# Kernel tuning notes

Hardware: AMD Instinct MI355X
Metric: run time of the kernel (lower is better)

## Reference

```python
import jax, jax.numpy as jnp
import numpy as np

B, T, M, D, H, DK, DV = 2, 1024, 1024, 1024, 16, 64, 64
R = 2 * T + M  # number of relative positions required by rel_shift path


def setup_inputs() -> dict:
    key = jax.random.key(0)
    ks = jax.random.split(key, 11)
    s = 0.02
    return {
        "inputs": jax.random.normal(ks[0], (B, T, D), jnp.float32),
        "attention_mask": jnp.ones((B, T, M + T), jnp.float32),
        "positional_encodings": jax.random.normal(ks[1], (R, D), jnp.float32),
        "memory": jax.random.normal(ks[2], (B, M, D), jnp.float32),
        "Wq": jax.random.normal(ks[3], (D, H * DK), jnp.float32) * s,
        "Wk": jax.random.normal(ks[4], (D, H * DK), jnp.float32) * s,
        "Wv": jax.random.normal(ks[5], (D, H * DV), jnp.float32) * s,
        "Wr": jax.random.normal(ks[6], (D, H * DK), jnp.float32) * s,
        "r_w_bias": jax.random.normal(ks[7], (H, DK), jnp.float32) * s,
        "r_r_bias": jax.random.normal(ks[8], (H, DK), jnp.float32) * s,
        "W_out": jax.random.normal(ks[9], (H * DV, D), jnp.float32) * s,
    }


def _rel_shift(m, attention_length):
    # m: [T_q, T_q + L] -> [T_q, L], TXL relative shift via reshape/slice
    tq, total = m.shape
    x = m.reshape(total, tq)[1:].reshape(tq, total - 1)
    return x[:, :attention_length]


def reference(inputs, attention_mask, positional_encodings, memory,
              Wq, Wk, Wv, Wr, r_w_bias, r_r_bias, W_out):
    b, t, d = inputs.shape
    values = jnp.concatenate([memory, inputs], axis=1)  # [B, L, D]
    L = values.shape[1]
    q = (inputs @ Wq).reshape(b, t, H, DK)
    k = (values @ Wk).reshape(b, L, H, DK)
    v = (values @ Wv).reshape(b, L, H, DV)
    rk = (positional_encodings @ Wr).reshape(-1, H, DK)  # [R, H, DK]
    # content + relative logits (TXL)
    content = jnp.einsum('bthd,bThd->bhtT', q + r_w_bias, k)        # [B,H,T,L]
    rel = jnp.einsum('bthd,rhd->bhtr', q + r_r_bias, rk)            # [B,H,T,R]
    rel = jax.vmap(jax.vmap(lambda m: _rel_shift(m, L)))(rel)       # [B,H,T,L]
    logits = (content + rel) * (DK ** -0.5)
    masked = logits - (1.0 - attention_mask[:, None, :, :]) * 1e30
    w = jax.nn.softmax(masked, axis=-1)
    attn = jnp.einsum('bhtT,bThd->bthd', w, v)                      # [B,T,H,DV]
    return attn.reshape(b, t, H * DV) @ W_out
```

## Files before the change

kernel.cpp:

```cpp
#include <hip/hip_runtime.h>
#include <hip/hip_fp16.h>
#include <stdint.h>

#define Bz 2
#define Tq 1024
#define Mm 1024
#define Hh 16
#define Ll 2048
#define Rr 3072

typedef __attribute__((ext_vector_type(8))) short bf16x8;
typedef __attribute__((ext_vector_type(4))) float f32x4;

typedef __attribute__((address_space(3))) uint8_t lds_u8_t;
typedef __attribute__((address_space(1))) uint8_t glb_u8_t;

__device__ __forceinline__ void gl2lds16(const void* g, void* l) {
  __builtin_amdgcn_global_load_lds((const glb_u8_t*)g, (lds_u8_t*)l, 16, 0, 0);
}

__device__ __forceinline__ unsigned short f2bf(float f) {
  unsigned int u = __builtin_bit_cast(unsigned int, f);
  u = u + 0x7fffu + ((u >> 16) & 1u);
  return (unsigned short)(u >> 16);
}
__device__ __forceinline__ float b2f(unsigned short s) {
  unsigned int u = ((unsigned int)s) << 16;
  return __builtin_bit_cast(float, u);
}

__global__ __launch_bounds__(256) void k_prep2(
    const float* __restrict__ x, const float* __restrict__ mem,
    const float* __restrict__ pos, const float* __restrict__ mask,
    const float* __restrict__ w0, const float* __restrict__ w1,
    const float* __restrict__ w2, const float* __restrict__ w3,
    const float* __restrict__ w4,
    unsigned short* __restrict__ vin, unsigned short* __restrict__ pb,
    unsigned short* __restrict__ mb,
    unsigned short* __restrict__ t0, unsigned short* __restrict__ t1,
    unsigned short* __restrict__ t2, unsigned short* __restrict__ t3,
    unsigned short* __restrict__ t4) {
  __shared__ float tile[64][65];
  int bid = blockIdx.x;
  if (bid < 4096) {
    int idx = bid * 256 + threadIdx.x;
    int e = idx << 2;
    int row = e >> 10, col = e & 1023;
    int b = row >> 11, l = row & 2047;
    const float* s = (l < Mm) ? (mem + (((size_t)b * Mm + l) << 10) + col)
                              : (x + (((size_t)b * Tq + (l - Mm)) << 10) + col);
    float4 v = *(const float4*)s;
    ushort4 o;
    o.x = f2bf(v.x); o.y = f2bf(v.y); o.z = f2bf(v.z); o.w = f2bf(v.w);
    *(ushort4*)(vin + e) = o;
  } else if (bid < 7168) {
    int idx = (bid - 4096) * 256 + threadIdx.x;
    int e = idx << 2;
    float4 v = *(const float4*)(pos + e);
    ushort4 t;
    t.x = f2bf(v.x); t.y = f2bf(v.y); t.z = f2bf(v.z); t.w = f2bf(v.w);
    *(ushort4*)(pb + e) = t;
  } else if (bid < 11264) {
    int idx = (bid - 7168) * 256 + threadIdx.x;
    int e = idx << 2;
    const float BIGM = 1.442695e30f;
    float4 v = *(const float4*)(mask + e);
    ushort4 t;
    t.x = f2bf((1.0f - v.x) * BIGM); t.y = f2bf((1.0f - v.y) * BIGM);
    t.z = f2bf((1.0f - v.z) * BIGM); t.w = f2bf((1.0f - v.w) * BIGM);
    *(ushort4*)(mb + e) = t;
  } else {
    int r3 = bid - 11264;
    int mz = r3 >> 8, rem = r3 & 255;
    const float* W;
    unsigned short* WT;
    switch (mz) {
      case 0: W = w0; WT = t0; break;
      case 1: W = w1; WT = t1; break;
      case 2: W = w2; WT = t2; break;
      case 3: W = w3; WT = t3; break;
      default: W = w4; WT = t4; break;
    }
    int k0 = (rem >> 4) * 64, n0 = (rem & 15) * 64;
    int tid = threadIdx.x;
    int rr = tid >> 4, c4 = (tid & 15) * 4;
#pragma unroll
    for (int it = 0; it < 4; ++it) {
      int r = rr + it * 16;
      float4 v = *(const float4*)(W + (size_t)(k0 + r) * 1024 + n0 + c4);
      tile[r][c4] = v.x; tile[r][c4 + 1] = v.y;
      tile[r][c4 + 2] = v.z; tile[r][c4 + 3] = v.w;
    }
    __syncthreads();
#pragma unroll
    for (int it = 0; it < 4; ++it) {
      int n = rr + it * 16;
      ushort4 o;
      o.x = f2bf(tile[c4 + 0][n]); o.y = f2bf(tile[c4 + 1][n]);
      o.z = f2bf(tile[c4 + 2][n]); o.w = f2bf(tile[c4 + 3][n]);
      *(ushort4*)(WT + (size_t)(n0 + n) * 1024 + k0 + c4) = o;
    }
  }
}

template <int RMAP>
__device__ __forceinline__ void gemm_pipe(const unsigned short* __restrict__ A,
                                          const unsigned short* __restrict__ Bt,
                                          int m0, int n0, unsigned short* As,
                                          unsigned short* Bs, f32x4 acc[4][4]) {
  const int tid = threadIdx.x;
  const int w = tid >> 6, lane = tid & 63;
  const int quad = lane >> 4, li = lane & 15;
  const int wr = w >> 1, wc = w & 1;
  f32x4 z = {0.f, 0.f, 0.f, 0.f};
#pragma unroll
  for (int mi = 0; mi < 4; ++mi)
#pragma unroll
    for (int ni = 0; ni < 4; ++ni) acc[mi][ni] = z;

  const int rs = lane >> 2;
  const int cs = lane & 3;

#pragma unroll
  for (int s = 0; s < 2; ++s) {
    int i = w * 2 + s;
    int r = i * 16 + rs;
    int c = cs ^ ((r >> 1) & 3);
    int ar = m0 + r;
    if (RMAP) ar = ar + 1024 + (ar & 1024);
    gl2lds16(A + (size_t)ar * 1024 + c * 8, (char*)As + i * 1024);
    gl2lds16(Bt + (size_t)(n0 + r) * 1024 + c * 8, (char*)Bs + i * 1024);
  }

  for (int k0 = 0; k0 < 1024; k0 += 32) {
    const int bo = ((k0 >> 5) & 1) * 8192;
    const int no = bo ^ 8192;
    __builtin_amdgcn_s_waitcnt(0x0F70);
    __syncthreads();
    if (k0 + 32 < 1024) {
#pragma unroll
      for (int s = 0; s < 2; ++s) {
        int i = w * 2 + s;
        int r = i * 16 + rs;
        int c = cs ^ ((r >> 1) & 3);
        int ar = m0 + r;
        if (RMAP) ar = ar + 1024 + (ar & 1024);
        gl2lds16(A + (size_t)ar * 1024 + k0 + 32 + c * 8,
                 (char*)As + no + i * 1024);
        gl2lds16(Bt + (size_t)(n0 + r) * 1024 + k0 + 32 + c * 8,
                 (char*)Bs + no + i * 1024);
      }
    }
    bf16x8 af[4], bfr[4];
#pragma unroll
    for (int mi = 0; mi < 4; ++mi) {
      int r = wr * 64 + mi * 16 + li;
      int ch = quad ^ ((r >> 1) & 3);
      af[mi] = *(const bf16x8*)((const char*)As + bo + r * 64 + ch * 16);
    }
#pragma unroll
    for (int ni = 0; ni < 4; ++ni) {
      int r = wc * 64 + ni * 16 + li;
      int ch = quad ^ ((r >> 1) & 3);
      bfr[ni] = *(const bf16x8*)((const char*)Bs + bo + r * 64 + ch * 16);
    }
#pragma unroll
    for (int mi = 0; mi < 4; ++mi)
#pragma unroll
      for (int ni = 0; ni < 4; ++ni)
        acc[mi][ni] = __builtin_amdgcn_mfma_f32_16x16x32_bf16(
            af[mi], bfr[ni], acc[mi][ni], 0, 0, 0);
  }
}

__global__ __launch_bounds__(256) void k_proj(
    const unsigned short* __restrict__ Vin, const unsigned short* __restrict__ Pb,
    const unsigned short* __restrict__ WqT, const unsigned short* __restrict__ WkT,
    const unsigned short* __restrict__ WvT, const unsigned short* __restrict__ WrT,
    unsigned short* __restrict__ qb, unsigned short* __restrict__ kb,
    unsigned short* __restrict__ vtb, unsigned short* __restrict__ rkb) {
  __shared__ unsigned short As[2 * 128 * 32];
  __shared__ unsigned short Bs[2 * 128 * 32];
  const int t = blockIdx.x;
  const int tid = threadIdx.x, w = tid >> 6, lane = tid & 63;
  const int quad = lane >> 4, li = lane & 15, wr = w >> 1, wc = w & 1;
  f32x4 acc[4][4];

  if (t < 256) {
    int m0 = (t >> 3) * 128, n0 = (t & 7) * 128;
    gemm_pipe<0>(Vin, WkT, m0, n0, As, Bs, acc);
#pragma unroll
    for (int mi = 0; mi < 4; ++mi)
#pragma unroll
      for (int ni = 0; ni < 4; ++ni)
#pragma unroll
        for (int reg = 0; reg < 4; ++reg) {
          int rrow = m0 + wr * 64 + mi * 16 + quad * 4 + reg;
          int cc = n0 + wc * 64 + ni * 16 + li;
          kb[(size_t)rrow * 1024 + cc] = f2bf(acc[mi][ni][reg]);
        }
  } else if (t < 512) {
    int tt = t - 256;
    int m0 = (tt >> 3) * 128, n0 = (tt & 7) * 128;
    gemm_pipe<0>(Vin, WvT, m0, n0, As, Bs, acc);
#pragma unroll
    for (int mi = 0; mi < 4; ++mi)
#pragma unroll
      for (int ni = 0; ni < 4; ++ni) {
        int r0 = m0 + wr * 64 + mi * 16 + quad * 4;
        int b = r0 >> 11, l0 = r0 & 2047;
        int cc = n0 + wc * 64 + ni * 16 + li;
        ushort4 o;
        o.x = f2bf(acc[mi][ni][0]); o.y = f2bf(acc[mi][ni][1]);
        o.z = f2bf(acc[mi][ni][2]); o.w = f2bf(acc[mi][ni][3]);
        *(ushort4*)(vtb + ((size_t)(b * 1024 + cc)) * Ll + l0) = o;
      }
  } else if (t < 640) {
    int tt = t - 512;
    int m0 = (tt >> 3) * 128, n0 = (tt & 7) * 128;
    gemm_pipe<1>(Vin, WqT, m0, n0, As, Bs, acc);
#pragma unroll
    for (int mi = 0; mi < 4; ++mi)
#pragma unroll
      for (int ni = 0; ni < 4; ++ni)
#pragma unroll
        for (int reg = 0; reg < 4; ++reg) {
          int rrow = m0 + wr * 64 + mi * 16 + quad * 4 + reg;
          int cc = n0 + wc * 64 + ni * 16 + li;
          qb[(size_t)rrow * 1024 + cc] = f2bf(acc[mi][ni][reg]);
        }
  } else {
    int tt = t - 640;
    int m0 = (tt >> 3) * 128, n0 = (tt & 7) * 128;
    gemm_pipe<0>(Pb, WrT, m0, n0, As, Bs, acc);
#pragma unroll
    for (int mi = 0; mi < 4; ++mi)
#pragma unroll
      for (int ni = 0; ni < 4; ++ni)
#pragma unroll
        for (int reg = 0; reg < 4; ++reg) {
          int rrow = m0 + wr * 64 + mi * 16 + quad * 4 + reg;
          int cc = n0 + wc * 64 + ni * 16 + li;
          rkb[(size_t)rrow * 1024 + cc] = f2bf(acc[mi][ni][reg]);
        }
  }
}

__global__ __launch_bounds__(256) void k_gemm_out64(
    const unsigned short* __restrict__ attnb, const unsigned short* __restrict__ WoT,
    float* __restrict__ out) {
  __shared__ unsigned short As[2 * 64 * 32];
  __shared__ unsigned short Bs[2 * 128 * 32];
  int m0 = blockIdx.x * 64, n0 = blockIdx.y * 128;
  const int tid = threadIdx.x, w = tid >> 6, lane = tid & 63;
  const int quad = lane >> 4, li = lane & 15, wr = w >> 1, wc = w & 1;
  f32x4 z = {0.f, 0.f, 0.f, 0.f};
  f32x4 acc[2][4];
#pragma unroll
  for (int mi = 0; mi < 2; ++mi)
#pragma unroll
    for (int ni = 0; ni < 4; ++ni) acc[mi][ni] = z;
  const int rs = lane >> 2, cs = lane & 3;

  {
    int r = w * 16 + rs;
    int c = cs ^ ((r >> 1) & 3);
    gl2lds16(attnb + (size_t)(m0 + r) * 1024 + c * 8, (char*)As + w * 1024);
  }
#pragma unroll
  for (int s = 0; s < 2; ++s) {
    int i = w * 2 + s;
    int r = i * 16 + rs;
    int c = cs ^ ((r >> 1) & 3);
    gl2lds16(WoT + (size_t)(n0 + r) * 1024 + c * 8, (char*)Bs + i * 1024);
  }

  for (int k0 = 0; k0 < 1024; k0 += 32) {
    const int boa = ((k0 >> 5) & 1) * 4096;
    const int bob = ((k0 >> 5) & 1) * 8192;
    __builtin_amdgcn_s_waitcnt(0x0F70);
    __syncthreads();
    if (k0 + 32 < 1024) {
      {
        int r = w * 16 + rs;
        int c = cs ^ ((r >> 1) & 3);
        gl2lds16(attnb + (size_t)(m0 + r) * 1024 + k0 + 32 + c * 8,
                 (char*)As + (boa ^ 4096) + w * 1024);
      }
#pragma unroll
      for (int s = 0; s < 2; ++s) {
        int i = w * 2 + s;
        int r = i * 16 + rs;
        int c = cs ^ ((r >> 1) & 3);
        gl2lds16(WoT + (size_t)(n0 + r) * 1024 + k0 + 32 + c * 8,
                 (char*)Bs + (bob ^ 8192) + i * 1024);
      }
    }
    bf16x8 af[2], bfr[4];
#pragma unroll
    for (int mi = 0; mi < 2; ++mi) {
      int r = wr * 32 + mi * 16 + li;
      int ch = quad ^ ((r >> 1) & 3);
      af[mi] = *(const bf16x8*)((const char*)As + boa + r * 64 + ch * 16);
    }
#pragma unroll
    for (int ni = 0; ni < 4; ++ni) {
      int r = wc * 64 + ni * 16 + li;
      int ch = quad ^ ((r >> 1) & 3);
      bfr[ni] = *(const bf16x8*)((const char*)Bs + bob + r * 64 + ch * 16);
    }
#pragma unroll
    for (int mi = 0; mi < 2; ++mi)
#pragma unroll
      for (int ni = 0; ni < 4; ++ni)
        acc[mi][ni] = __builtin_amdgcn_mfma_f32_16x16x32_bf16(
            af[mi], bfr[ni], acc[mi][ni], 0, 0, 0);
  }
#pragma unroll
  for (int mi = 0; mi < 2; ++mi)
#pragma unroll
    for (int ni = 0; ni < 4; ++ni)
#pragma unroll
      for (int reg = 0; reg < 4; ++reg) {
        int rrow = m0 + wr * 32 + mi * 16 + quad * 4 + reg;
        int cc = n0 + wc * 64 + ni * 16 + li;
        out[(size_t)rrow * 1024 + cc] = acc[mi][ni][reg];
      }
}

__global__ __launch_bounds__(512, 4) void k_attn(
    const unsigned short* __restrict__ qb, const float* __restrict__ rwb,
    const float* __restrict__ rrb,
    const unsigned short* __restrict__ kb, const unsigned short* __restrict__ vt,
    const unsigned short* __restrict__ rkb, const unsigned short* __restrict__ mb,
    unsigned short* __restrict__ attnb) {
  __shared__ __align__(16) uint8_t lds[75776];

  const int tid = threadIdx.x;
  const int w = tid >> 6, lane = tid & 63;
  const int quad = lane >> 4, li = lane & 15;
  const int wq = w & 3, grp = w >> 2;
  const int srow = lane >> 3, scs = lane & 7;
  const int flat = blockIdx.x + 16 * blockIdx.y + 256 * blockIdx.z;
  const int qt = (flat >> 3) & 15;
  const int g = 4 * (flat & 7) + (flat >> 7);
  const int h = g & 15, b = g >> 4;
  const int t0blk = qt * 64;
  const int t0w = t0blk + wq * 16;
  const int rboff = 48 - 16 * wq;
  const int rbase0 = Tq - t0blk - 63;
  const int jbase = grp * 1024;

  unsigned short* KS = (unsigned short*)(lds + grp * 8192);
  unsigned short* VS = (unsigned short*)(lds + 16384 + grp * 8192);
  unsigned short* RS = (unsigned short*)(lds + 32768 + grp * 16384);
  unsigned short* pw = (unsigned short*)(lds + 65536 + w * 1280);
  float* red = (float*)(lds + 32768);

  const unsigned short* kbase = kb + ((size_t)(b * Ll + jbase) * Hh + h) * 64;
  const unsigned short* vbase = vt + ((size_t)((b * Hh + h) * 64)) * Ll + jbase;
  const unsigned short* rkbase = rkb + (size_t)h * 64;
  const unsigned short* mrow = mb + ((size_t)(b * Tq + t0w + li)) * Ll + jbase;

  bf16x8 aqw[2], aqr[2];
  {
    const unsigned short* p1 = qb + ((size_t)((b * Tq + t0w + li) * Hh + h)) * 64;
#pragma unroll
    for (int ks = 0; ks < 2; ++ks) {
      bf16x8 qf = *(const bf16x8*)(p1 + ks * 32 + quad * 8);
      const float* wp = rwb + h * 64 + ks * 32 + quad * 8;
      const float* rp = rrb + h * 64 + ks * 32 + quad * 8;
      float4 w0 = *(const float4*)wp, w1 = *(const float4*)(wp + 4);
      float4 r0 = *(const float4*)rp, r1 = *(const float4*)(rp + 4);
      float wv[8] = {w0.x, w0.y, w0.z, w0.w, w1.x, w1.y, w1.z, w1.w};
      float rv[8] = {r0.x, r0.y, r0.z, r0.w, r1.x, r1.y, r1.z, r1.w};
#pragma unroll
      for (int i2 = 0; i2 < 8; ++i2) {
        float qv = b2f((unsigned short)qf[i2]);
        aqw[ks][i2] = (short)f2bf(qv + wv[i2]);
        aqr[ks][i2] = (short)f2bf(qv + rv[i2]);
      }
    }
  }

  f32x4 z = {0.f, 0.f, 0.f, 0.f};
  f32x4 o[4];
  o[0] = z; o[1] = z; o[2] = z; o[3] = z;
  f32x4 ol = z;
  bf16x8 nmv = {0, 0, 0, 0, 0, 0, 0, 0};

  const float SC = 0.125f * 1.4426950408889634f;
  const short oneb = 0x3F80;
  const bf16x8 onesf = {oneb, oneb, oneb, oneb, oneb, oneb, oneb, oneb};

  int srcl[4];
#pragma unroll
  for (int reg = 0; reg < 4; ++reg) {
    int row = quad * 4 + reg;
    srcl[reg] = (lane & 48) + ((li + row + 1) & 15);
  }

  auto finish = [&](const unsigned short* VsP, bf16x8 mv) {
    bf16x8 sv = *(const bf16x8*)(pw + li * 40 + quad * 8);
    bf16x8 apv;
#pragma unroll
    for (int i2 = 0; i2 < 8; ++i2) {
      float sf = __half2float(__builtin_bit_cast(__half, (unsigned short)sv[i2]));
      float mvf = b2f((unsigned short)mv[i2]);
      float p = exp2f(sf * SC - mvf);
      apv[i2] = (short)f2bf(p);
    }
    __builtin_amdgcn_s_setprio(1);
    ol = __builtin_amdgcn_mfma_f32_16x16x32_bf16(apv, onesf, ol, 0, 0, 0);
#pragma unroll
    for (int nt = 0; nt < 4; ++nt) {
      int dv = nt * 16 + li;
      int ch = quad ^ (dv & 3);
      bf16x8 vf = *(const bf16x8*)(VsP + dv * 32 + ch * 8);
      o[nt] = __builtin_amdgcn_mfma_f32_16x16x32_bf16(apv, vf, o[nt], 0, 0, 0);
    }
    __builtin_amdgcn_s_setprio(0);
  };

#pragma unroll
  for (int pass = 0; pass < 3; ++pass) {
    int u = pass * 32 + wq * 8 + srow;
    int gr = rbase0 + jbase + u;
    if (gr > Rr - 1) gr = Rr - 1;
    int c = scs ^ srow;
    gl2lds16(rkbase + (size_t)gr * 1024 + c * 8, RS + (pass * 32 + wq * 8) * 64);
  }
  {
    int r = wq * 8 + srow;
    int c = scs ^ srow;
    gl2lds16(kbase + (size_t)r * 1024 + c * 8, KS + wq * 512);
  }

  for (int jt = 0; jt < 32; ++jt) {
    const int jloc = jt * 32;
    __builtin_amdgcn_s_waitcnt(0x0F70);
    __syncthreads();
    if (jt < 31) {
      {
        int r = wq * 8 + srow;
        int c = scs ^ srow;
        gl2lds16(kbase + (size_t)(jloc + 32 + r) * 1024 + c * 8,
                 KS + (((jt + 1) & 1) * 2048) + wq * 512);
      }
      {
        int u = jloc + 96 + wq * 8 + srow;
        int gr = rbase0 + jbase + u;
        if (gr > Rr - 1) gr = Rr - 1;
        int c = scs ^ srow;
        gl2lds16(rkbase + (size_t)gr * 1024 + c * 8,
                 RS + ((jloc + 96 + wq * 8) & 127) * 64);
      }
    }
    {
      int dv = wq * 16 + (lane >> 2);
      int c = (lane & 3) ^ (dv & 3);
      gl2lds16(vbase + (size_t)dv * Ll + jloc + c * 8,
               VS + ((jt & 1) * 2048) + wq * 512);
    }
    asm volatile("" ::: "memory");
    const unsigned short* KsC = KS + (jt & 1) * 2048;
    f32x4 sc[2];
    sc[0] = z; sc[1] = z;
    __builtin_amdgcn_s_setprio(1);
#pragma unroll
    for (int ks = 0; ks < 2; ++ks)
#pragma unroll
      for (int nt = 0; nt < 2; ++nt) {
        int j = nt * 16 + li;
        int ch = (ks * 4 + quad) ^ (j & 7);
        bf16x8 kf = *(const bf16x8*)(KsC + j * 64 + ch * 8);
        sc[nt] = __builtin_amdgcn_mfma_f32_16x16x32_bf16(aqw[ks], kf, sc[nt], 0, 0, 0);
      }
    f32x4 bd[3];
    bd[0] = z; bd[1] = z; bd[2] = z;
#pragma unroll
    for (int ks = 0; ks < 2; ++ks)
#pragma unroll
      for (int nt = 0; nt < 3; ++nt) {
        int pr = (rboff + nt * 16 + li + jloc) & 127;
        int ch = (ks * 4 + quad) ^ (pr & 7);
        bf16x8 rf = *(const bf16x8*)(RS + pr * 64 + ch * 8);
        bd[nt] = __builtin_amdgcn_mfma_f32_16x16x32_bf16(aqr[ks], rf, bd[nt], 0, 0, 0);
      }
    __builtin_amdgcn_s_setprio(0);
    if (jt > 0) finish(VS + ((jt - 1) & 1) * 2048, nmv);
    nmv = *(const bf16x8*)(mrow + jloc + quad * 8);
    float rot[2][4];
#pragma unroll
    for (int nt = 0; nt < 2; ++nt)
#pragma unroll
      for (int reg = 0; reg < 4; ++reg)
        rot[nt][reg] = __shfl(sc[nt][reg], srcl[reg], 64);
#pragma unroll
    for (int nt = 0; nt < 3; ++nt)
#pragma unroll
      for (int reg = 0; reg < 4; ++reg) {
        int row = quad * 4 + reg;
        int jj = nt * 16 + li + row - 15;
        int nthi = (nt > 1) ? 0 : nt;
        int ntlo = (nt == 0) ? 0 : (nt - 1);
        float val = ((li + row) >= 15) ? rot[nthi][reg] : rot[ntlo][reg];
        float s = val + bd[nt][reg];
        if ((unsigned)jj < 32u)
          pw[row * 40 + jj] = __builtin_bit_cast(unsigned short, __float2half(s));
      }
  }
  __builtin_amdgcn_s_waitcnt(0x0F70);
  __syncthreads();
  finish(VS + 2048, nmv);

  if (grp == 1) {
    float* rp = red + (size_t)(wq * 64 + lane) * 20;
#pragma unroll
    for (int nt = 0; nt < 4; ++nt)
#pragma unroll
      for (int reg = 0; reg < 4; ++reg) rp[nt * 4 + reg] = o[nt][reg];
#pragma unroll
    for (int reg = 0; reg < 4; ++reg) rp[16 + reg] = ol[reg];
  }
  __syncthreads();
  if (grp == 0) {
    const float* rp = red + (size_t)(wq * 64 + lane) * 20;
    float inv[4];
#pragma unroll
    for (int reg = 0; reg < 4; ++reg) inv[reg] = 1.0f / (ol[reg] + rp[16 + reg]);
#pragma unroll
    for (int nt = 0; nt < 4; ++nt)
#pragma unroll
      for (int reg = 0; reg < 4; ++reg) {
        int trow = t0w + quad * 4 + reg;
        float val = (o[nt][reg] + rp[nt * 4 + reg]) * inv[reg];
        attnb[((size_t)(b * Tq + trow)) * 1024 + h * 64 + nt * 16 + li] = f2bf(val);
      }
  }
}

extern "C" void kernel_launch(void* const* d_in, const int* in_sizes, int n_in,
                              void* d_out, int out_size, void* d_ws, size_t ws_size,
                              hipStream_t stream) {
  const float* x = (const float*)d_in[0];
  const float* mask = (const float*)d_in[1];
  const float* pos = (const float*)d_in[2];
  const float* mem = (const float*)d_in[3];
  const float* Wq = (const float*)d_in[4];
  const float* Wk = (const float*)d_in[5];
  const float* Wv = (const float*)d_in[6];
  const float* Wr = (const float*)d_in[7];
  const float* rwb = (const float*)d_in[8];
  const float* rrb = (const float*)d_in[9];
  const float* Wo = (const float*)d_in[10];
  float* out = (float*)d_out;

  uint8_t* ws = (uint8_t*)d_ws;
  const size_t MB = 1024 * 1024;
  unsigned short* Vinb = (unsigned short*)(ws + 0);
  unsigned short* WqT = (unsigned short*)(ws + 8 * MB);
  unsigned short* WkT = (unsigned short*)(ws + 10 * MB);
  unsigned short* WvT = (unsigned short*)(ws + 12 * MB);
  unsigned short* WrT = (unsigned short*)(ws + 14 * MB);
  unsigned short* WoT = (unsigned short*)(ws + 16 * MB);
  unsigned short* Pb = (unsigned short*)(ws + 18 * MB);
  unsigned short* qb = (unsigned short*)(ws + 24 * MB);
  unsigned short* kb = (unsigned short*)(ws + 32 * MB);
  unsigned short* vtb = (unsigned short*)(ws + 40 * MB);
  unsigned short* rkb = (unsigned short*)(ws + 48 * MB);
  unsigned short* mbb = (unsigned short*)(ws + 54 * MB);
  unsigned short* attnb = (unsigned short*)(ws + 19 * MB);

  hipLaunchKernelGGL(k_prep2, dim3(12544), dim3(256), 0, stream,
                     x, mem, pos, mask, Wq, Wk, Wv, Wr, Wo,
                     Vinb, Pb, mbb, WqT, WkT, WvT, WrT, WoT);
  hipLaunchKernelGGL(k_proj, dim3(832), dim3(256), 0, stream,
                     Vinb, Pb, WqT, WkT, WvT, WrT, qb, kb, vtb, rkb);
  hipLaunchKernelGGL(k_attn, dim3(16, 16, 2), dim3(512), 0, stream,
                     qb, rwb, rrb, kb, vtb, rkb, mbb, attnb);
  hipLaunchKernelGGL(k_gemm_out64, dim3(32, 8), dim3(256), 0, stream,
                     attnb, WoT, out);
}
```

Before: 252.7 us.

## Load relative-key fragments directly from global memory, shrinking LDS for occupancy

Removes the LDS ring buffer for the relative-position keys and has each lane load its rk MFMA fragments straight from global memory every iteration. This frees about 32KB of LDS, so the launch-bounds occupancy hint is raised from 4 to 6 blocks. The V tile swizzle is also changed to reduce LDS bank conflicts. In exchange, the rk loads are now uncoalesced global reads issued right before the MFMAs that use them, with no prefetch, which can expose memory latency. Each wave also re-reads overlapping rows that were previously shared through LDS.

```diff
diff --git a/kernel.cpp b/kernel.cpp
--- a/kernel.cpp
+++ b/kernel.cpp
@@ -328,13 +328,13 @@
       }
 }
 
-__global__ __launch_bounds__(512, 4) void k_attn(
+__global__ __launch_bounds__(512, 6) void k_attn(
     const unsigned short* __restrict__ qb, const float* __restrict__ rwb,
     const float* __restrict__ rrb,
     const unsigned short* __restrict__ kb, const unsigned short* __restrict__ vt,
     const unsigned short* __restrict__ rkb, const unsigned short* __restrict__ mb,
     unsigned short* __restrict__ attnb) {
-  __shared__ __align__(16) uint8_t lds[75776];
+  __shared__ __align__(16) uint8_t lds[43008];
 
   const int tid = threadIdx.x;
   const int w = tid >> 6, lane = tid & 63;
@@ -353,9 +353,8 @@
 
   unsigned short* KS = (unsigned short*)(lds + grp * 8192);
   unsigned short* VS = (unsigned short*)(lds + 16384 + grp * 8192);
-  unsigned short* RS = (unsigned short*)(lds + 32768 + grp * 16384);
-  unsigned short* pw = (unsigned short*)(lds + 65536 + w * 1280);
-  float* red = (float*)(lds + 32768);
+  unsigned short* pw = (unsigned short*)(lds + 32768 + w * 1280);
+  float* red = (float*)(lds + 0);
 
   const unsigned short* kbase = kb + ((size_t)(b * Ll + jbase) * Hh + h) * 64;
   const unsigned short* vbase = vt + ((size_t)((b * Hh + h) * 64)) * Ll + jbase;
@@ -415,21 +414,13 @@
 #pragma unroll
     for (int nt = 0; nt < 4; ++nt) {
       int dv = nt * 16 + li;
-      int ch = quad ^ (dv & 3);
+      int ch = quad ^ ((dv >> 1) & 3);
       bf16x8 vf = *(const bf16x8*)(VsP + dv * 32 + ch * 8);
       o[nt] = __builtin_amdgcn_mfma_f32_16x16x32_bf16(apv, vf, o[nt], 0, 0, 0);
     }
     __builtin_amdgcn_s_setprio(0);
   };
 
-#pragma unroll
-  for (int pass = 0; pass < 3; ++pass) {
-    int u = pass * 32 + wq * 8 + srow;
-    int gr = rbase0 + jbase + u;
-    if (gr > Rr - 1) gr = Rr - 1;
-    int c = scs ^ srow;
-    gl2lds16(rkbase + (size_t)gr * 1024 + c * 8, RS + (pass * 32 + wq * 8) * 64);
-  }
   {
     int r = wq * 8 + srow;
     int c = scs ^ srow;
@@ -441,26 +432,26 @@
     __builtin_amdgcn_s_waitcnt(0x0F70);
     __syncthreads();
     if (jt < 31) {
-      {
-        int r = wq * 8 + srow;
-        int c = scs ^ srow;
-        gl2lds16(kbase + (size_t)(jloc + 32 + r) * 1024 + c * 8,
-                 KS + (((jt + 1) & 1) * 2048) + wq * 512);
-      }
-      {
-        int u = jloc + 96 + wq * 8 + srow;
-        int gr = rbase0 + jbase + u;
-        if (gr > Rr - 1) gr = Rr - 1;
-        int c = scs ^ srow;
-        gl2lds16(rkbase + (size_t)gr * 1024 + c * 8,
-                 RS + ((jloc + 96 + wq * 8) & 127) * 64);
-      }
+      int r = wq * 8 + srow;
+      int c = scs ^ srow;
+      gl2lds16(kbase + (size_t)(jloc + 32 + r) * 1024 + c * 8,
+               KS + (((jt + 1) & 1) * 2048) + wq * 512);
     }
     {
       int dv = wq * 16 + (lane >> 2);
-      int c = (lane & 3) ^ (dv & 3);
+      int c = (lane & 3) ^ ((dv >> 1) & 3);
       gl2lds16(vbase + (size_t)dv * Ll + jloc + c * 8,
                VS + ((jt & 1) * 2048) + wq * 512);
+    }
+    bf16x8 rfv[2][3];
+#pragma unroll
+    for (int nt = 0; nt < 3; ++nt) {
+      int gr = rbase0 + jbase + jloc + rboff + nt * 16 + li;
+      if (gr > Rr - 1) gr = Rr - 1;
+      const unsigned short* rp = rkbase + (size_t)gr * 1024;
+#pragma unroll
+      for (int ks = 0; ks < 2; ++ks)
+        rfv[ks][nt] = *(const bf16x8*)(rp + ks * 32 + quad * 8);
     }
     asm volatile("" ::: "memory");
     const unsigned short* KsC = KS + (jt & 1) * 2048;
@@ -481,12 +472,9 @@
 #pragma unroll
     for (int ks = 0; ks < 2; ++ks)
 #pragma unroll
-      for (int nt = 0; nt < 3; ++nt) {
-        int pr = (rboff + nt * 16 + li + jloc) & 127;
-        int ch = (ks * 4 + quad) ^ (pr & 7);
-        bf16x8 rf = *(const bf16x8*)(RS + pr * 64 + ch * 8);
-        bd[nt] = __builtin_amdgcn_mfma_f32_16x16x32_bf16(aqr[ks], rf, bd[nt], 0, 0, 0);
-      }
+      for (int nt = 0; nt < 3; ++nt)
+        bd[nt] = __builtin_amdgcn_mfma_f32_16x16x32_bf16(aqr[ks], rfv[ks][nt],
+                                                         bd[nt], 0, 0, 0);
     __builtin_amdgcn_s_setprio(0);
     if (jt > 0) finish(VS + ((jt - 1) & 1) * 2048, nmv);
     nmv = *(const bf16x8*)(mrow + jloc + quad * 8);
```

Measured after the change: 449.1 us. +77.7%, slower.
